# Optimization experiments

Hardware: AMD Instinct MI355X
Metric: run time of the kernel (lower is better)

## Reference

```python
import jax, jax.numpy as jnp
import numpy as np

B, T, EMB, HS = 4, 4096, 1024, 64
BASE = 10000.0


def rope_angles(T, hs, base=BASE):
    # theta_i = base^(-2i/hs), freqs[t, i] = t * theta_i  -> (T, hs//2)
    inv = 1.0 / (base ** (2.0 * jnp.arange(hs // 2, dtype=jnp.float32) / hs))
    return jnp.arange(T, dtype=jnp.float32)[:, None] * inv[None, :]


def apply_rope(x, cos, sin):
    # x: (B, T, D); pairs are interleaved (even, odd) like torch.view_as_complex
    xr = x.reshape(*x.shape[:-1], -1, 2)
    xe, xo = xr[..., 0], xr[..., 1]
    re = xe * cos - xo * sin
    im = xe * sin + xo * cos
    return jnp.stack([re, im], axis=-1).reshape(x.shape)


def setup_inputs() -> dict:
    key = jax.random.key(0)
    kx, kq, kk, kv = jax.random.split(key, 4)
    s = 1.0 / np.sqrt(EMB)
    return {
        "x": jax.random.normal(kx, (B, T, EMB), jnp.float32),
        "Wq": jax.random.normal(kq, (HS, EMB), jnp.float32) * s,
        "Wk": jax.random.normal(kk, (HS, EMB), jnp.float32) * s,
        "Wv": jax.random.normal(kv, (HS, EMB), jnp.float32) * s,
    }


def reference(x, Wq, Wk, Wv):
    Tlen = x.shape[1]
    ang = rope_angles(Tlen, HS)          # (T, HS//2)
    cos, sin = jnp.cos(ang), jnp.sin(ang)
    q = x @ Wq.T                          # (B, T, HS)
    k = x @ Wk.T
    v = x @ Wv.T
    q = apply_rope(q, cos, sin)
    k = apply_rope(k, cos, sin)
    scores = jnp.einsum("bqd,bkd->bqk", q, k) * (HS ** -0.5)
    causal = jnp.tril(jnp.ones((Tlen, Tlen), dtype=bool))
    scores = jnp.where(causal[None], scores, -jnp.inf)
    w = jax.nn.softmax(scores, axis=-1)   # dropout in eval mode: identity
    return jnp.einsum("bqk,bkd->bqd", w, v)
```

## Files before the change

kernel.cpp:

```cpp
#include <hip/hip_runtime.h>

typedef __bf16 bf16x8 __attribute__((ext_vector_type(8)));
typedef __bf16 bf16x4 __attribute__((ext_vector_type(4)));
typedef float f32x4 __attribute__((ext_vector_type(4)));
typedef float f32x16 __attribute__((ext_vector_type(16)));
typedef unsigned int u32;

#define T_LEN 4096

__device__ __forceinline__ f32x4 mfma16(bf16x8 a, bf16x8 b, f32x4 c) {
    return __builtin_amdgcn_mfma_f32_16x16x32_bf16(a, b, c, 0, 0, 0);
}
__device__ __forceinline__ f32x16 mfma32(bf16x8 a, bf16x8 b, f32x16 c) {
    return __builtin_amdgcn_mfma_f32_32x32x16_bf16(a, b, c, 0, 0, 0);
}
__device__ __forceinline__ u32 packbf(float lo, float hi) {
    union { __bf16 e[2]; u32 w; } u;
    u.e[0] = (__bf16)lo; u.e[1] = (__bf16)hi;
    return u.w;
}
__device__ __forceinline__ f32x16 zero16() {
    f32x16 z;
    #pragma unroll
    for (int i = 0; i < 16; i++) z[i] = 0.f;
    return z;
}

__global__ __launch_bounds__(256) void convert_w_kernel(
    const float* __restrict__ Wq, const float* __restrict__ Wk,
    const float* __restrict__ Wv, __bf16* __restrict__ wb)
{
    int i = blockIdx.x * 256 + threadIdx.x;
    int m = i >> 14, off = (i & 16383) << 2;
    const float* s = (m == 0 ? Wq : (m == 1 ? Wk : Wv)) + off;
    float4 f = *(const float4*)s;
    bf16x4 h = { (__bf16)f.x, (__bf16)f.y, (__bf16)f.z, (__bf16)f.w };
    *(bf16x4*)(wb + (m << 16) + off) = h;
}

__global__ __launch_bounds__(512, 2) void proj_kernel(
    const float* __restrict__ x, const __bf16* __restrict__ wb,
    __bf16* __restrict__ qfb, __bf16* __restrict__ kfb, __bf16* __restrict__ vfb)
{
    __shared__ __bf16 smem[36864];
    __bf16 (*xs)[64][72]  = (__bf16(*)[64][72])smem;
    __bf16 (*wl)[192][72] = (__bf16(*)[192][72])(smem + 9216);
    __bf16* stage = smem;

    const int tid  = threadIdx.x;
    const int wave = tid >> 6, lane = tid & 63;
    const int l15 = lane & 15, l4 = lane >> 4;
    const int wm = wave >> 2, wn = wave & 3;
    const size_t m0 = (size_t)blockIdx.x * 64;
    const int srow = tid >> 3, scp = (tid & 7) * 8;

    f32x4 acc[2][3];
    #pragma unroll
    for (int a = 0; a < 2; a++)
        #pragma unroll
        for (int bn = 0; bn < 3; bn++) acc[a][bn] = (f32x4){0.f, 0.f, 0.f, 0.f};

    const float* xsrc = x + (m0 + srow) * 1024 + scp;

    float4 rx0, rx1;
    bf16x8 rw[3];

    rx0 = *(const float4*)(xsrc);
    rx1 = *(const float4*)(xsrc + 4);
    #pragma unroll
    for (int j = 0; j < 3; j++)
        rw[j] = *(const bf16x8*)(wb + (size_t)(srow + j * 64) * 1024 + scp);
    {
        bf16x8 h = {(__bf16)rx0.x, (__bf16)rx0.y, (__bf16)rx0.z, (__bf16)rx0.w,
                    (__bf16)rx1.x, (__bf16)rx1.y, (__bf16)rx1.z, (__bf16)rx1.w};
        *(bf16x8*)&xs[0][srow][scp] = h;
        #pragma unroll
        for (int j = 0; j < 3; j++)
            *(bf16x8*)&wl[0][srow + j * 64][scp] = rw[j];
    }
    __syncthreads();

    for (int t = 0; t < 16; t++) {
        const int cur = t & 1;
        if (t < 15) {
            const int k0 = (t + 1) * 64;
            rx0 = *(const float4*)(xsrc + k0);
            rx1 = *(const float4*)(xsrc + k0 + 4);
            #pragma unroll
            for (int j = 0; j < 3; j++)
                rw[j] = *(const bf16x8*)(wb + (size_t)(srow + j * 64) * 1024 + k0 + scp);
        }
        bf16x8 af[2][2], bfr[3][2];
        #pragma unroll
        for (int mf = 0; mf < 2; mf++)
            #pragma unroll
            for (int c = 0; c < 2; c++)
                af[mf][c] = *(const bf16x8*)&xs[cur][wm * 32 + mf * 16 + l15][c * 32 + l4 * 8];
        #pragma unroll
        for (int nf = 0; nf < 3; nf++)
            #pragma unroll
            for (int c = 0; c < 2; c++)
                bfr[nf][c] = *(const bf16x8*)&wl[cur][wn * 48 + nf * 16 + l15][c * 32 + l4 * 8];
        #pragma unroll
        for (int mf = 0; mf < 2; mf++)
            #pragma unroll
            for (int nf = 0; nf < 3; nf++)
                #pragma unroll
                for (int c = 0; c < 2; c++)
                    acc[mf][nf] = mfma16(af[mf][c], bfr[nf][c], acc[mf][nf]);
        if (t < 15) {
            bf16x8 h = {(__bf16)rx0.x, (__bf16)rx0.y, (__bf16)rx0.z, (__bf16)rx0.w,
                        (__bf16)rx1.x, (__bf16)rx1.y, (__bf16)rx1.z, (__bf16)rx1.w};
            *(bf16x8*)&xs[cur ^ 1][srow][scp] = h;
            #pragma unroll
            for (int j = 0; j < 3; j++)
                *(bf16x8*)&wl[cur ^ 1][srow + j * 64][scp] = rw[j];
        }
        __syncthreads();
    }

    const int tq0 = (int)(m0 & 4095);
    #pragma unroll
    for (int nf = 0; nf < 3; nf++) {
        int n = wn * 48 + nf * 16 + l15;
        #pragma unroll
        for (int mf = 0; mf < 2; mf++) {
            #pragma unroll
            for (int r = 0; r < 4; r++) {
                int row64 = wm * 32 + mf * 16 + l4 * 4 + r;
                int tile = row64 >> 5, rr = row64 & 31;
                int tb = tile * 6144;
                float val = acc[mf][nf][r];
                float partner = __shfl_xor(val, 1);
                if (n < 128) {
                    int i = (n & 63) >> 1;
                    float ang = (float)(tq0 + row64)
                              * __builtin_exp2f((float)i * (-13.287712379549449f / 32.f));
                    float sn, cs;
                    __sincosf(ang, &sn, &cs);
                    float res = (n & 1) ? (partner * sn + val * cs)
                                        : (val * cs - partner * sn);
                    if (n < 64) {
                        res *= 0.180336884f;
                        int d = n;
                        stage[tb + (d >> 4) * 512
                              + (rr + ((d >> 3) & 1) * 32) * 8 + (d & 7)] = (__bf16)res;
                    } else {
                        int d = n - 64;
                        int l31i = ((rr >> 2) & 1) * 16 + ((rr >> 4) & 1) * 8
                                 + ((rr >> 3) & 1) * 4 + (rr & 3);
                        stage[tb + 2048 + (d >> 4) * 512
                              + (l31i + ((d >> 3) & 1) * 32) * 8 + (d & 7)] = (__bf16)res;
                    }
                } else {
                    int d = n - 128;
                    int cc = ((d >> 5) << 1) | (rr >> 4);
                    stage[tb + 4096 + cc * 512
                          + ((d & 31) + ((rr >> 3) & 1) * 32) * 8 + (rr & 7)]
                        = (__bf16)val;
                }
            }
        }
    }
    __syncthreads();
    {
        const size_t bbase = (size_t)(m0 >> 12) * 262144;
        const size_t tbase = (size_t)((m0 & 4095) >> 5) * 2048;
        #pragma unroll
        for (int tile = 0; tile < 2; tile++) {
            const int tb = tile * 6144;
            const size_t go = bbase + tbase + (size_t)tile * 2048 + tid * 4;
            bf16x4 q4 = *(const bf16x4*)&stage[tb + tid * 4];
            bf16x4 k4 = *(const bf16x4*)&stage[tb + 2048 + tid * 4];
            bf16x4 v4 = *(const bf16x4*)&stage[tb + 4096 + tid * 4];
            *(bf16x4*)(qfb + go) = q4;
            *(bf16x4*)(kfb + go) = k4;
            *(bf16x4*)(vfb + go) = v4;
        }
    }
}

__global__ __launch_bounds__(1024) void flash_kernel(
    const __bf16* __restrict__ qfb, const __bf16* __restrict__ kfb,
    const __bf16* __restrict__ vfb, float* __restrict__ out)
{
    __shared__ float ods[16][32][36];
    __shared__ float mls[2][16][32];

    const int tid = threadIdx.x;
    const int wave = tid >> 6, lane = tid & 63;
    const int l31 = lane & 31, h = lane >> 5;
    const int xcd = blockIdx.x & 7;
    const int b = xcd >> 1;
    const int p = ((blockIdx.x >> 3) << 1) | (xcd & 1);

    const __bf16* qb_b = qfb + (size_t)b * 262144;
    const __bf16* kb_b = kfb + (size_t)b * 262144;
    const __bf16* vb_b = vfb + (size_t)b * 262144;

    #pragma unroll 1
    for (int half = 0; half < 2; half++) {
        const int jt = half ? p : 127 - p;
        const int q0 = jt * 32;
        const int qg = q0 + l31;

        const __bf16* qp = qb_b + (size_t)jt * 2048 + lane * 8;
        bf16x8 qf[4];
        #pragma unroll
        for (int dc = 0; dc < 4; dc++) qf[dc] = *(const bf16x8*)(qp + dc * 512);

        float m = 16.f, l = 0.f;
        f32x16 o0 = zero16(), o1 = zero16();
        const int nt = jt + 1;

        #pragma unroll 1
        for (int kt = wave; kt < nt; kt += 16) {
            const int kc0 = kt << 5;
            const __bf16* kr = kb_b + (size_t)kt * 2048 + lane * 8;
            bf16x8 kf0 = *(const bf16x8*)(kr);
            bf16x8 kf1 = *(const bf16x8*)(kr + 512);
            bf16x8 kf2 = *(const bf16x8*)(kr + 1024);
            bf16x8 kf3 = *(const bf16x8*)(kr + 1536);
            const __bf16* vr = vb_b + (size_t)kt * 2048 + lane * 8;
            bf16x8 vf00 = *(const bf16x8*)(vr);
            bf16x8 vf01 = *(const bf16x8*)(vr + 512);
            bf16x8 vf10 = *(const bf16x8*)(vr + 1024);
            bf16x8 vf11 = *(const bf16x8*)(vr + 1536);
            f32x16 s = zero16();
            __builtin_amdgcn_s_setprio(1);
            s = mfma32(kf0, qf[0], s);
            s = mfma32(kf1, qf[1], s);
            s = mfma32(kf2, qf[2], s);
            s = mfma32(kf3, qf[3], s);
            __builtin_amdgcn_s_setprio(0);
            if (kt == jt) {
                #pragma unroll
                for (int r = 0; r < 16; r++) {
                    int pioff = ((r >> 2) & 1) * 16 + 8 * h + (r >> 3) * 4 + (r & 3);
                    if (kc0 + pioff > qg) s[r] = -1e30f;
                }
            }
            float tm[8];
            #pragma unroll
            for (int i = 0; i < 8; i++) tm[i] = fmaxf(s[2 * i], s[2 * i + 1]);
            #pragma unroll
            for (int i = 0; i < 4; i++) tm[i] = fmaxf(tm[i], tm[i + 4]);
            float tmax = fmaxf(fmaxf(tm[0], tm[1]), fmaxf(tm[2], tm[3]));
            float ts[4] = {0.f, 0.f, 0.f, 0.f};
            #pragma unroll
            for (int r = 0; r < 16; r++) {
                float e = __builtin_exp2f(s[r] - m);
                s[r] = e;
                ts[r & 3] += e;
            }
            float lsum = (ts[0] + ts[1]) + (ts[2] + ts[3]);
            float lsum_p = __shfl_xor(lsum, 32);
            float tmax_p = __shfl_xor(tmax, 32);
            union { u32 w[4]; bf16x8 v; } pf[2];
            #pragma unroll
            for (int cg = 0; cg < 2; cg++) {
                pf[cg].w[0] = packbf(s[4 * cg + 0],  s[4 * cg + 1]);
                pf[cg].w[1] = packbf(s[4 * cg + 2],  s[4 * cg + 3]);
                pf[cg].w[2] = packbf(s[4 * cg + 8],  s[4 * cg + 9]);
                pf[cg].w[3] = packbf(s[4 * cg + 10], s[4 * cg + 11]);
            }
            __builtin_amdgcn_s_setprio(1);
            o0 = mfma32(vf00, pf[0].v, o0);
            o0 = mfma32(vf01, pf[1].v, o0);
            o1 = mfma32(vf10, pf[0].v, o1);
            o1 = mfma32(vf11, pf[1].v, o1);
            __builtin_amdgcn_s_setprio(0);
            l += lsum + lsum_p;
            float tmx = fmaxf(tmax, tmax_p);
            if (!__all(tmx <= m + 8.f)) {
                const float mnew = fmaxf(m, tmx);
                const float alpha = __builtin_exp2f(m - mnew);
                m = mnew;
                l *= alpha;
                #pragma unroll
                for (int r = 0; r < 16; r++) { o0[r] *= alpha; o1[r] *= alpha; }
            }
        }

        const int q = tid >> 5, dcm = tid & 31;
        #pragma unroll
        for (int c2 = 0; c2 < 4; c2++) {
            f32x4 w0 = {o0[4 * c2], o0[4 * c2 + 1], o0[4 * c2 + 2], o0[4 * c2 + 3]};
            *(f32x4*)&ods[wave][l31][8 * c2 + 4 * h] = w0;
        }
        if (h == 0) {
            mls[0][wave][l31] = (wave < nt) ? m : -1e30f;
            mls[1][wave][l31] = l;
        }
        __syncthreads();
        float M = -1e30f;
        #pragma unroll
        for (int s2 = 0; s2 < 16; s2++) M = fmaxf(M, mls[0][s2][q]);
        float w16[16], L = 0.f;
        #pragma unroll
        for (int s2 = 0; s2 < 16; s2++) {
            float ws = __builtin_exp2f(mls[0][s2][q] - M);
            w16[s2] = ws;
            L += ws * mls[1][s2][q];
        }
        const float invL = 1.f / L;
        float accA = 0.f;
        #pragma unroll
        for (int s2 = 0; s2 < 16; s2++) accA += w16[s2] * ods[s2][q][dcm];
        out[((size_t)b * T_LEN + q0 + q) * 64 + dcm] = accA * invL;
        __syncthreads();
        #pragma unroll
        for (int c2 = 0; c2 < 4; c2++) {
            f32x4 w1 = {o1[4 * c2], o1[4 * c2 + 1], o1[4 * c2 + 2], o1[4 * c2 + 3]};
            *(f32x4*)&ods[wave][l31][8 * c2 + 4 * h] = w1;
        }
        __syncthreads();
        float accB = 0.f;
        #pragma unroll
        for (int s2 = 0; s2 < 16; s2++) accB += w16[s2] * ods[s2][q][dcm];
        out[((size_t)b * T_LEN + q0 + q) * 64 + 32 + dcm] = accB * invL;
        __syncthreads();
    }
}

extern "C" void kernel_launch(void* const* d_in, const int* in_sizes, int n_in,
                              void* d_out, int out_size, void* d_ws, size_t ws_size,
                              hipStream_t stream)
{
    const float* x  = (const float*)d_in[0];
    const float* Wq = (const float*)d_in[1];
    const float* Wk = (const float*)d_in[2];
    const float* Wv = (const float*)d_in[3];
    float* out = (float*)d_out;

    __bf16* qfb = (__bf16*)d_ws;
    __bf16* kfb = qfb + 1048576;
    __bf16* vfb = kfb + 1048576;
    __bf16* wb  = vfb + 1048576;

    convert_w_kernel<<<192, 256, 0, stream>>>(Wq, Wk, Wv, wb);
    proj_kernel<<<256, 512, 0, stream>>>(x, wb, qfb, kfb, vfb);
    flash_kernel<<<256, 1024, 0, stream>>>(qfb, kfb, vfb, out);
}
```

Before: 54.24 us.

## Prelayout weights as swizzled K-tiles and stream them via direct global-to-LDS loads

The weight conversion kernel now writes bf16 weights in per-K-step tiles with an XOR swizzle on 16-byte chunks, so each 64-wide K slice is contiguous. The projection kernel fetches these tiles with global_load_lds straight into shared memory, skipping the register round-trip and dropping the padded LDS layout. Reads use the matching swizzle to avoid bank conflicts. This cuts VGPR pressure and LDS store instructions in the GEMM loop. The risk is async-load ordering relative to __syncthreads and a more complex addressing scheme.

```diff
diff --git a/kernel.cpp b/kernel.cpp
--- a/kernel.cpp
+++ b/kernel.cpp
@@ -25,26 +25,37 @@
     for (int i = 0; i < 16; i++) z[i] = 0.f;
     return z;
 }
+__device__ __forceinline__ void gload_lds16(const __bf16* g, __bf16* l) {
+    __builtin_amdgcn_global_load_lds(
+        (const __attribute__((address_space(1))) u32*)g,
+        (__attribute__((address_space(3))) u32*)l, 16, 0, 0);
+}
 
 __global__ __launch_bounds__(256) void convert_w_kernel(
     const float* __restrict__ Wq, const float* __restrict__ Wk,
-    const float* __restrict__ Wv, __bf16* __restrict__ wb)
+    const float* __restrict__ Wv, __bf16* __restrict__ wf)
 {
-    int i = blockIdx.x * 256 + threadIdx.x;
-    int m = i >> 14, off = (i & 16383) << 2;
-    const float* s = (m == 0 ? Wq : (m == 1 ? Wk : Wv)) + off;
-    float4 f = *(const float4*)s;
-    bf16x4 h = { (__bf16)f.x, (__bf16)f.y, (__bf16)f.z, (__bf16)f.w };
-    *(bf16x4*)(wb + (m << 16) + off) = h;
+    int t = blockIdx.x * 256 + threadIdx.x;
+    int ks = t / 1536;
+    int rem = t - ks * 1536;
+    int n = rem >> 3, g = rem & 7;
+    const float* src = (n < 64 ? Wq : (n < 128 ? Wk : Wv))
+                     + (size_t)(n & 63) * 1024 + ks * 64 + g * 8;
+    float4 f0 = *(const float4*)src;
+    float4 f1 = *(const float4*)(src + 4);
+    bf16x8 h = {(__bf16)f0.x, (__bf16)f0.y, (__bf16)f0.z, (__bf16)f0.w,
+                (__bf16)f1.x, (__bf16)f1.y, (__bf16)f1.z, (__bf16)f1.w};
+    int chunk = n * 8 + (g ^ (n & 7));
+    *(bf16x8*)(wf + (size_t)ks * 12288 + chunk * 8) = h;
 }
 
 __global__ __launch_bounds__(512, 2) void proj_kernel(
-    const float* __restrict__ x, const __bf16* __restrict__ wb,
+    const float* __restrict__ x, const __bf16* __restrict__ wf,
     __bf16* __restrict__ qfb, __bf16* __restrict__ kfb, __bf16* __restrict__ vfb)
 {
-    __shared__ __bf16 smem[36864];
-    __bf16 (*xs)[64][72]  = (__bf16(*)[64][72])smem;
-    __bf16 (*wl)[192][72] = (__bf16(*)[192][72])(smem + 9216);
+    __shared__ __bf16 smem[33792];
+    __bf16 (*xs)[64][72] = (__bf16(*)[64][72])smem;
+    __bf16* wl = smem + 9216;
     __bf16* stage = smem;
 
     const int tid  = threadIdx.x;
@@ -63,20 +74,17 @@
     const float* xsrc = x + (m0 + srow) * 1024 + scp;
 
     float4 rx0, rx1;
-    bf16x8 rw[3];
 
     rx0 = *(const float4*)(xsrc);
     rx1 = *(const float4*)(xsrc + 4);
-    #pragma unroll
-    for (int j = 0; j < 3; j++)
-        rw[j] = *(const bf16x8*)(wb + (size_t)(srow + j * 64) * 1024 + scp);
     {
         bf16x8 h = {(__bf16)rx0.x, (__bf16)rx0.y, (__bf16)rx0.z, (__bf16)rx0.w,
                     (__bf16)rx1.x, (__bf16)rx1.y, (__bf16)rx1.z, (__bf16)rx1.w};
         *(bf16x8*)&xs[0][srow][scp] = h;
-        #pragma unroll
-        for (int j = 0; j < 3; j++)
-            *(bf16x8*)&wl[0][srow + j * 64][scp] = rw[j];
+        __bf16* wdst = wl + wave * 512;
+        #pragma unroll
+        for (int i = 0; i < 3; i++)
+            gload_lds16(wf + (size_t)i * 4096 + (size_t)tid * 8, wdst + i * 4096);
     }
     __syncthreads();
 
@@ -86,35 +94,35 @@
             const int k0 = (t + 1) * 64;
             rx0 = *(const float4*)(xsrc + k0);
             rx1 = *(const float4*)(xsrc + k0 + 4);
-            #pragma unroll
-            for (int j = 0; j < 3; j++)
-                rw[j] = *(const bf16x8*)(wb + (size_t)(srow + j * 64) * 1024 + k0 + scp);
-        }
-        bf16x8 af[2][2], bfr[3][2];
+            const __bf16* wsrc = wf + (size_t)(t + 1) * 12288;
+            __bf16* wdst = wl + (cur ^ 1) * 12288 + wave * 512;
+            #pragma unroll
+            for (int i = 0; i < 3; i++)
+                gload_lds16(wsrc + (size_t)i * 4096 + (size_t)tid * 8, wdst + i * 4096);
+        }
+        const __bf16* wcur = wl + cur * 12288;
+        bf16x8 af[2][2];
         #pragma unroll
         for (int mf = 0; mf < 2; mf++)
             #pragma unroll
             for (int c = 0; c < 2; c++)
                 af[mf][c] = *(const bf16x8*)&xs[cur][wm * 32 + mf * 16 + l15][c * 32 + l4 * 8];
         #pragma unroll
-        for (int nf = 0; nf < 3; nf++)
-            #pragma unroll
-            for (int c = 0; c < 2; c++)
-                bfr[nf][c] = *(const bf16x8*)&wl[cur][wn * 48 + nf * 16 + l15][c * 32 + l4 * 8];
-        #pragma unroll
-        for (int mf = 0; mf < 2; mf++)
-            #pragma unroll
-            for (int nf = 0; nf < 3; nf++)
+        for (int nf = 0; nf < 3; nf++) {
+            const int n = wn * 48 + nf * 16 + l15;
+            const int sw = n & 7;
+            #pragma unroll
+            for (int c = 0; c < 2; c++) {
+                bf16x8 bw = *(const bf16x8*)(wcur + (size_t)(n * 8 + ((c * 4 + l4) ^ sw)) * 8);
                 #pragma unroll
-                for (int c = 0; c < 2; c++)
-                    acc[mf][nf] = mfma16(af[mf][c], bfr[nf][c], acc[mf][nf]);
+                for (int mf = 0; mf < 2; mf++)
+                    acc[mf][nf] = mfma16(af[mf][c], bw, acc[mf][nf]);
+            }
+        }
         if (t < 15) {
             bf16x8 h = {(__bf16)rx0.x, (__bf16)rx0.y, (__bf16)rx0.z, (__bf16)rx0.w,
                         (__bf16)rx1.x, (__bf16)rx1.y, (__bf16)rx1.z, (__bf16)rx1.w};
             *(bf16x8*)&xs[cur ^ 1][srow][scp] = h;
-            #pragma unroll
-            for (int j = 0; j < 3; j++)
-                *(bf16x8*)&wl[cur ^ 1][srow + j * 64][scp] = rw[j];
         }
         __syncthreads();
     }
@@ -336,9 +344,9 @@
     __bf16* qfb = (__bf16*)d_ws;
     __bf16* kfb = qfb + 1048576;
     __bf16* vfb = kfb + 1048576;
-    __bf16* wb  = vfb + 1048576;
-
-    convert_w_kernel<<<192, 256, 0, stream>>>(Wq, Wk, Wv, wb);
-    proj_kernel<<<256, 512, 0, stream>>>(x, wb, qfb, kfb, vfb);
+    __bf16* wf  = vfb + 1048576;
+
+    convert_w_kernel<<<96, 256, 0, stream>>>(Wq, Wk, Wv, wf);
+    proj_kernel<<<256, 512, 0, stream>>>(x, wf, qfb, kfb, vfb);
     flash_kernel<<<256, 1024, 0, stream>>>(qfb, kfb, vfb, out);
 }
```

Result: no change. 54.16 us (-0.1%).
